# Kernel tuning notes

Measured on AMD Instinct MI355X. Metric: run time of the kernel, lower is better.

Reference implementation:

```python
import jax, jax.numpy as jnp
import numpy as np

INPUT_SIZE = 32
UNITS = 1024
T = 8192
N_MODULES = 2
INPUT_SCALING = 1.0
SPECTRAL_RADIUS = 0.99
LEAKY = 0.5
C_IN = 10
C_REC = 10


def _sparse_input_kernel(rng, M, N, C):
    # each row (input dim) projects to C random reservoir units, U(-1,1)
    W = np.zeros((M, N), dtype=np.float32)
    for i in range(M):
        idx = rng.choice(N, size=C, replace=False)
        W[i, idx] = rng.uniform(-1.0, 1.0, size=C).astype(np.float32)
    return W


def _sparse_recurrent_kernel(rng, M, C):
    # each column (unit) receives input from C random units, U(-1,1)
    W = np.zeros((M, M), dtype=np.float32)
    for i in range(M):
        idx = rng.choice(M, size=C, replace=False)
        W[idx, i] = rng.uniform(-1.0, 1.0, size=C).astype(np.float32)
    return W


def _make_recurrent(rng, M, leaky, rho):
    W = _sparse_recurrent_kernel(rng, M, C_REC)
    I = np.eye(M, dtype=np.float32)
    if leaky == 1:
        e = np.linalg.eigvals(W)
        W = W * (rho / np.max(np.abs(e)))
    else:
        W = W * leaky + I * (1.0 - leaky)
        e = np.linalg.eigvals(W)
        W = W * (rho / np.max(np.abs(e)))
        W = (W + I * (leaky - 1.0)) * (1.0 / leaky)
    return W.astype(np.float32)


def setup_inputs() -> dict:
    key = jax.random.key(0)
    rng = np.random.default_rng(0)
    u = jax.random.normal(key, (1, T, INPUT_SIZE), dtype=jnp.float32)
    # module 0: input_size -> units; module 1: units -> units
    kernel0 = jnp.asarray(_sparse_input_kernel(rng, INPUT_SIZE, UNITS, C_IN) * INPUT_SCALING)
    rec0 = jnp.asarray(_make_recurrent(rng, UNITS, LEAKY, SPECTRAL_RADIUS))
    bias0 = jnp.asarray(rng.uniform(-1.0, 1.0, size=UNITS).astype(np.float32))
    kernel1 = jnp.asarray(_sparse_input_kernel(rng, UNITS, UNITS, C_IN) * INPUT_SCALING)
    rec1 = jnp.asarray(_make_recurrent(rng, UNITS, LEAKY, SPECTRAL_RADIUS))
    bias1 = jnp.asarray(rng.uniform(-1.0, 1.0, size=UNITS).astype(np.float32))
    return {"u": u, "kernel0": kernel0, "rec0": rec0, "bias0": bias0,
            "kernel1": kernel1, "rec1": rec1, "bias1": bias1}


def _run_reservoir(u, K, W, b):
    # u: [B, T, in]; leaky-integrator ESN scan over time
    def step(h, ut):
        out = jnp.tanh(ut @ K + b + h @ W)
        h_new = h * (1.0 - LEAKY) + out * LEAKY
        return h_new, h_new
    h0 = jnp.zeros((u.shape[0], K.shape[1]), dtype=u.dtype)
    _, hs = jax.lax.scan(step, h0, jnp.swapaxes(u, 0, 1))  # [T, B, units]
    return jnp.swapaxes(hs, 0, 1)  # [B, T, units]


def reference(u, kernel0, rec0, bias0, kernel1, rec1, bias1):
    hs0 = _run_reservoir(u, kernel0, rec0, bias0)
    hs1 = _run_reservoir(hs0, kernel1, rec1, bias1)
    # deep reservoir output: concatenation of all module state sequences
    return jnp.concatenate([hs0, hs1], axis=-1)  # [1, T, 2*UNITS]
```

## Files before the change

kernel.cpp:

```cpp
#include <hip/hip_runtime.h>
#include <math.h>

typedef unsigned int uint;

#define T_STEPS 8192
#define R_CAP 10
#define K1_CAP 32
#define K0_CAP 6

__global__ __launch_bounds__(256) void prep_extract(
    const float* __restrict__ k0w, const float* __restrict__ r0w,
    const float* __restrict__ r1w, const float* __restrict__ k1w,
    float* __restrict__ r0vr, uint* __restrict__ r0ur, float* __restrict__ d0r,
    float* __restrict__ r1vr, uint* __restrict__ r1ur, float* __restrict__ d1r,
    float* __restrict__ k1vr, uint* __restrict__ k1ur, int* __restrict__ c1r,
    float* __restrict__ k0vr, uint* __restrict__ k0ur, int* __restrict__ c0r)
{
    int tid = blockIdx.x * 256 + threadIdx.x;
    int task = tid >> 10, j = tid & 1023;

    if (task <= 1) {
        const float* W = task ? r1w : r0w;
        float* vr = task ? r1vr : r0vr;
        uint*  ur = task ? r1ur : r0ur;
        float* dr = task ? d1r  : d0r;
        float diag = 0.f; int c = 0;
#pragma unroll 4
        for (int i = 0; i < 1024; ++i) {
            float v = W[i * 1024 + j];
            if (i == j) diag = v;
            else if (v != 0.f && c < R_CAP) {
                vr[j * R_CAP + c] = v; ur[j * R_CAP + c] = (uint)i; ++c;
            }
        }
        for (; c < R_CAP; ++c) { vr[j * R_CAP + c] = 0.f; ur[j * R_CAP + c] = 0u; }
        dr[j] = diag;
    } else if (task == 2) {
        int c = 0;
#pragma unroll 4
        for (int i = 0; i < 1024; ++i) {
            float v = k1w[i * 1024 + j];
            if (v != 0.f && c < K1_CAP) {
                k1vr[j * K1_CAP + c] = v; k1ur[j * K1_CAP + c] = (uint)i; ++c;
            }
        }
        c1r[j] = c;
        for (int q = c; q < K1_CAP; ++q) { k1vr[j * K1_CAP + q] = 0.f; k1ur[j * K1_CAP + q] = 0u; }
    } else {
        int c = 0;
        for (int i = 0; i < 32; ++i) {
            float v = k0w[i * 1024 + j];
            if (v != 0.f && c < K0_CAP) {
                k0vr[j * K0_CAP + c] = v; k0ur[j * K0_CAP + c] = (uint)i; ++c;
            }
        }
        c0r[j] = c;
        for (int q = c; q < K0_CAP; ++q) { k0vr[j * K0_CAP + q] = 0.f; k0ur[j * K0_CAP + q] = 0u; }
    }
}

__global__ __launch_bounds__(1024) void prep_slots(
    const float* __restrict__ r0vr, const uint* __restrict__ r0ur,
    const float* __restrict__ r1vr, const uint* __restrict__ r1ur,
    const float* __restrict__ k1vr, const uint* __restrict__ k1ur, const int* __restrict__ c1r,
    const float* __restrict__ k0vr, const uint* __restrict__ k0ur, const int* __restrict__ c0r,
    uint* __restrict__ Gr0a, float* __restrict__ Gr0v, int* __restrict__ Gcr0,
    uint* __restrict__ Gr1a, float* __restrict__ Gr1v, int* __restrict__ Gcr1,
    uint* __restrict__ Gk1a, float* __restrict__ Gk1v, int* __restrict__ Fc1,
    uint* __restrict__ Gk0a, float* __restrict__ Gk0v, int* __restrict__ Fc0,
    int* __restrict__ Fu1, int* __restrict__ Linv1)
{
    __shared__ int lc1[1024];
    __shared__ unsigned short sl1[1024];
    const int j = threadIdx.x;
    const int c1j = c1r[j], c0j = c0r[j];
    lc1[j] = c1j;
    __syncthreads();
    int s1 = 0;
#pragma unroll 4
    for (int i = 0; i < 1024; ++i) {
        int a = lc1[i]; s1 += (a < c1j) || (a == c1j && i < j);
    }
    sl1[j] = (unsigned short)s1;
    __syncthreads();

    {
        int n = 0;
        for (int k = 0; k < R_CAP; ++k) {
            float v = r0vr[j * R_CAP + k];
            uint  u = r0ur[j * R_CAP + k];
            Gr0v[j * R_CAP + k] = v;
            Gr0a[j * R_CAP + k] = (v != 0.f) ? (u << 2) : 0u;
            if (v != 0.f) n = k + 1;
        }
        Gcr0[j] = n;
        for (int k = 0; k < K0_CAP; ++k) {
            Gk0v[j * K0_CAP + k] = k0vr[j * K0_CAP + k];
            Gk0a[j * K0_CAP + k] = (k < c0j) ? (k0ur[j * K0_CAP + k] << 2) : 0u;
        }
        Fc0[j] = c0j;
    }
    {
        int n = 0;
        for (int k = 0; k < R_CAP; ++k) {
            float v = r1vr[j * R_CAP + k];
            uint  u = r1ur[j * R_CAP + k];
            Gr1v[s1 * R_CAP + k] = v;
            Gr1a[s1 * R_CAP + k] = (v != 0.f) ? (8192u + ((uint)sl1[u] << 2)) : 8192u;
            if (v != 0.f) n = k + 1;
        }
        Gcr1[s1] = n;
        for (int k = 0; k < K1_CAP; ++k) {
            Gk1v[s1 * K1_CAP + k] = k1vr[j * K1_CAP + k];
            Gk1a[s1 * K1_CAP + k] = (k < c1j) ? (k1ur[j * K1_CAP + k] << 2) : 0u;
        }
        Fc1[s1] = c1j; Fu1[s1] = j;
    }
    Linv1[j] = s1;
}

__global__ __launch_bounds__(256) void prep_greedy(
    const uint* __restrict__ Gr0a, const float* __restrict__ Gr0v, const int* __restrict__ Gcr0,
    const uint* __restrict__ Gr1a, const float* __restrict__ Gr1v, const int* __restrict__ Gcr1,
    const uint* __restrict__ Gk1a, const float* __restrict__ Gk1v, const int* __restrict__ Fc1,
    const uint* __restrict__ Gk0a, const float* __restrict__ Gk0v, const int* __restrict__ Fc0,
    float* __restrict__ Fr0v, uint* __restrict__ Fr0a,
    float* __restrict__ Fr1v, uint* __restrict__ Fr1a,
    float* __restrict__ Fk1v, uint* __restrict__ Fk1a,
    float* __restrict__ Fk0v, uint* __restrict__ Fk0a)
{
    __shared__ uint  ea[4][64][32];
    __shared__ float ev[4][64][32];
    __shared__ int   bl[4][64];
    const int wv   = threadIdx.x >> 6;
    const int lane = threadIdx.x & 63;
    const int half = (lane >> 5) * 32;
    const int gw   = blockIdx.x * 4 + wv;
    const int task = gw >> 4;
    const int col  = (gw & 15) * 64 + lane;

    const uint* ga; const float* gv; const int* gc; int cap;
    float* fv; uint* fa;
    if (task == 0)      { ga = Gr0a; gv = Gr0v; gc = Gcr0; cap = R_CAP;  fv = Fr0v; fa = Fr0a; }
    else if (task == 1) { ga = Gr1a; gv = Gr1v; gc = Gcr1; cap = R_CAP;  fv = Fr1v; fa = Fr1a; }
    else if (task == 2) { ga = Gk1a; gv = Gk1v; gc = Fc1;  cap = K1_CAP; fv = Fk1v; fa = Fk1a; }
    else                { ga = Gk0a; gv = Gk0v; gc = Fc0;  cap = K0_CAP; fv = Fk0v; fa = Fk0a; }

    const int cnt = gc[col];
    for (int s = 0; s < cap; ++s) {
        ea[wv][lane][s] = ga[col * cap + s];
        ev[wv][lane][s] = gv[col * cap + s];
    }
    __syncthreads();

    for (int slot = 0; slot < 32; ++slot) {
        bl[wv][lane] = 0;
        __syncthreads();
        int pick = -1;
        const bool active = (slot < cap) && (slot < cnt);
        for (int rnd = 0; rnd < 4; ++rnd) {
            if (active && pick < 0) {
                int best = slot, bload = 1 << 30;
                for (int e = slot; e < cnt; ++e) {
                    int b  = (int)((ea[wv][lane][e] >> 2) & 31u);
                    int ld = bl[wv][half + b];
                    if (ld < bload) { bload = ld; best = e; }
                }
                int bb = (int)((ea[wv][lane][best] >> 2) & 31u);
                if (rnd == 3) {
                    atomicAdd(&bl[wv][half + bb], 1); pick = best;
                } else {
                    int old = atomicAdd(&bl[wv][half + bb], 1);
                    if (old >= 1) atomicSub(&bl[wv][half + bb], 1);
                    else pick = best;
                }
            }
            __syncthreads();
        }
        if (active && pick > slot) {
            uint  ta = ea[wv][lane][slot]; ea[wv][lane][slot] = ea[wv][lane][pick]; ea[wv][lane][pick] = ta;
            float tv = ev[wv][lane][slot]; ev[wv][lane][slot] = ev[wv][lane][pick]; ev[wv][lane][pick] = tv;
        }
        __syncthreads();
    }

    for (int s = 0; s < cap; ++s) fv[col * cap + s] = ev[wv][lane][s];
    for (int p = 0; p < cap / 2; ++p)
        fa[col * (cap / 2) + p] = (ea[wv][lane][2 * p] & 0xffffu) | (ea[wv][lane][2 * p + 1] << 16);
}

__device__ __forceinline__ float fast_tanh(float x) {
    float ax = fabsf(x);
    float e  = __expf(-2.0f * ax);
    float r  = __builtin_amdgcn_rcpf(1.0f + e);
    float t  = (1.0f - e) * r;
    return copysignf(t, x);
}

#define LD(A) (*(const float*)(smem + (A)))

#define STEP(P, UOFF, DO1)                                                     \
  {                                                                            \
    float xa = __builtin_fmaf(d0, h0j, b0), xb = 0.f, xc = 0.f, xd = 0.f;      \
    {                                                                          \
      uint p0 = r0a[0], p1 = r0a[1], p2 = r0a[2], p3 = r0a[3], p4 = r0a[4];    \
      xa += r0v[0] * LD((p0 & 0xffffu) + (P) * 4096u);                         \
      xb += r0v[1] * LD((p0 >> 16)     + (P) * 4096u);                         \
      xc += r0v[2] * LD((p1 & 0xffffu) + (P) * 4096u);                         \
      xd += r0v[3] * LD((p1 >> 16)     + (P) * 4096u);                         \
      xa += r0v[4] * LD((p2 & 0xffffu) + (P) * 4096u);                         \
      xb += r0v[5] * LD((p2 >> 16)     + (P) * 4096u);                         \
      xc += r0v[6] * LD((p3 & 0xffffu) + (P) * 4096u);                         \
      xd += r0v[7] * LD((p3 >> 16)     + (P) * 4096u);                         \
      xa += r0v[8] * LD((p4 & 0xffffu) + (P) * 4096u);                         \
      xb += r0v[9] * LD((p4 >> 16)     + (P) * 4096u);                         \
    }                                                                          \
    _Pragma("unroll")                                                          \
    for (int kc = 0; kc < K0_CAP; kc += 2) {                                   \
      if (kc < k0m) {                                                          \
        uint pr = k0a[kc >> 1];                                                \
        xc += k0v[kc]     * LD((pr & 0xffffu) + (UOFF));                       \
        xd += k0v[kc + 1] * LD((pr >> 16)     + (UOFF));                       \
      }                                                                        \
    }                                                                          \
    float o0  = fast_tanh((xa + xb) + (xc + xd));                              \
    float h0n = 0.5f * (h0j + o0);                                             \
    ((float*)(smem + (1 - (P)) * 4096u))[j] = h0n;                             \
    *o0p = h0n; o0p += 2048;                                                   \
    __syncthreads();                                                           \
    float g1 = 0.f;                                                            \
    if (DO1) g1 = LD(8192u + (P) * 4096u + l1off);                             \
    float ya = __builtin_fmaf(d1, h1j, b1), yb = 0.f, yc = 0.f, yd = 0.f;      \
    _Pragma("unroll")                                                          \
    for (int kc = 0; kc < K1_CAP; kc += 4) {                                   \
      if (kc < k1m) {                                                          \
        uint pa = k1a[kc >> 1], pb = k1a[(kc >> 1) + 1];                       \
        ya += k1v[kc]     * LD((pa & 0xffffu) + (1 - (P)) * 4096u);            \
        yb += k1v[kc + 1] * LD((pa >> 16)     + (1 - (P)) * 4096u);            \
        yc += k1v[kc + 2] * LD((pb & 0xffffu) + (1 - (P)) * 4096u);            \
        yd += k1v[kc + 3] * LD((pb >> 16)     + (1 - (P)) * 4096u);            \
      }                                                                        \
    }                                                                          \
    {                                                                          \
      uint p0 = r1a[0], p1 = r1a[1], p2 = r1a[2], p3 = r1a[3], p4 = r1a[4];    \
      ya += r1v[0] * LD((p0 & 0xffffu) + (P) * 4096u);                         \
      yb += r1v[1] * LD((p0 >> 16)     + (P) * 4096u);                         \
      yc += r1v[2] * LD((p1 & 0xffffu) + (P) * 4096u);                         \
      yd += r1v[3] * LD((p1 >> 16)     + (P) * 4096u);                         \
      ya += r1v[4] * LD((p2 & 0xffffu) + (P) * 4096u);                         \
      yb += r1v[5] * LD((p2 >> 16)     + (P) * 4096u);                         \
      yc += r1v[6] * LD((p3 & 0xffffu) + (P) * 4096u);                         \
      yd += r1v[7] * LD((p3 >> 16)     + (P) * 4096u);                         \
      ya += r1v[8] * LD((p4 & 0xffffu) + (P) * 4096u);                         \
      yb += r1v[9] * LD((p4 >> 16)     + (P) * 4096u);                         \
    }                                                                          \
    if (DO1) { *o1p = g1; o1p += 2048; }                                       \
    float o1  = fast_tanh((ya + yb) + (yc + yd));                              \
    float h1n = 0.5f * (h1j + o1);                                             \
    ((float*)(smem + 8192u + (1 - (P)) * 4096u))[j] = h1n;                     \
    h0j = h0n; h1j = h1n;                                                      \
  }

__global__ __launch_bounds__(1024, 4) void reservoir_main(
    const float* __restrict__ u,
    const float* __restrict__ bias0, const float* __restrict__ bias1,
    const float* __restrict__ d0r, const float* __restrict__ d1r,
    const float* __restrict__ Fr0v, const uint* __restrict__ Fr0a,
    const float* __restrict__ Fr1v, const uint* __restrict__ Fr1a,
    const float* __restrict__ Fk1v, const uint* __restrict__ Fk1a,
    const float* __restrict__ Fk0v, const uint* __restrict__ Fk0a,
    const int* __restrict__ Fc1, const int* __restrict__ Fc0,
    const int* __restrict__ Fu1, const int* __restrict__ Linv1,
    float* __restrict__ out)
{
    __shared__ __align__(16) char smem[24576];
    const int j = threadIdx.x;

    float r0v[R_CAP], r1v[R_CAP], k1v[K1_CAP], k0v[K0_CAP];
    uint  r0a[R_CAP / 2], r1a[R_CAP / 2], k1a[K1_CAP / 2], k0a[K0_CAP / 2];
#pragma unroll
    for (int k = 0; k < R_CAP; ++k) { r0v[k] = Fr0v[j * R_CAP + k]; r1v[k] = Fr1v[j * R_CAP + k]; }
#pragma unroll
    for (int k = 0; k < R_CAP / 2; ++k) { r0a[k] = Fr0a[j * (R_CAP / 2) + k]; r1a[k] = Fr1a[j * (R_CAP / 2) + k]; }
#pragma unroll
    for (int k = 0; k < K1_CAP; ++k) k1v[k] = Fk1v[j * K1_CAP + k];
#pragma unroll
    for (int k = 0; k < K1_CAP / 2; ++k) k1a[k] = Fk1a[j * (K1_CAP / 2) + k];
#pragma unroll
    for (int k = 0; k < K0_CAP; ++k) k0v[k] = Fk0v[j * K0_CAP + k];
#pragma unroll
    for (int k = 0; k < K0_CAP / 2; ++k) k0a[k] = Fk0a[j * (K0_CAP / 2) + k];

    const int u1 = Fu1[j];
    const float b0 = bias0[j],  d0 = d0r[j];
    const float b1 = bias1[u1], d1 = d1r[u1];
    const uint l1off = (uint)(Linv1[j] << 2);
    float* o0p = out + j;
    float* o1p = out + 1024 + j;

    int k1m = Fc1[j], k0m = Fc0[j];
#pragma unroll
    for (int s = 32; s >= 1; s >>= 1) {
        int a = __shfl_xor(k1m, s, 64); k1m = a > k1m ? a : k1m;
        int b = __shfl_xor(k0m, s, 64); k0m = b > k0m ? b : k0m;
    }
    k1m = __builtin_amdgcn_readfirstlane((k1m + 3) & ~3);
    k0m = __builtin_amdgcn_readfirstlane((k0m + 1) & ~1);

    ((float*)(smem        ))[j] = 0.f;
    ((float*)(smem +  4096))[j] = 0.f;
    ((float*)(smem +  8192))[j] = 0.f;
    ((float*)(smem + 12288))[j] = 0.f;
    float h0j = 0.f, h1j = 0.f;

    {
        ((float*)(smem + 16384))[j]        = u[j];
        ((float*)(smem + 16384))[1024 + j] = u[1024 + j];
        __syncthreads();
        STEP(0, 16384u, 0)
        STEP(1, 16384u + 128u, 1)
    }
    for (int t = 2; t < T_STEPS; t += 2) {
        if ((t & 63) == 0) {
            ((float*)(smem + 16384))[j]        = u[t * 32 + j];
            ((float*)(smem + 16384))[1024 + j] = u[t * 32 + 1024 + j];
            __syncthreads();
        }
        uint uoff = 16384u + (uint)((t & 63) << 7);
        STEP(0, uoff, 1)
        STEP(1, uoff + 128u, 1)
    }
    __syncthreads();
    *o1p = LD(8192u + l1off);
}

extern "C" void kernel_launch(void* const* d_in, const int* in_sizes, int n_in,
                              void* d_out, int out_size, void* d_ws, size_t ws_size,
                              hipStream_t stream) {
    const float* u   = (const float*)d_in[0];
    const float* k0w = (const float*)d_in[1];
    const float* r0w = (const float*)d_in[2];
    const float* b0  = (const float*)d_in[3];
    const float* k1w = (const float*)d_in[4];
    const float* r1w = (const float*)d_in[5];
    const float* b1  = (const float*)d_in[6];
    float* out = (float*)d_out;

    char* w = (char*)d_ws;
    float* r0vr = (float*)w; w += 1024 * R_CAP * 4;
    uint*  r0ur = (uint*)w;  w += 1024 * R_CAP * 4;
    float* d0r  = (float*)w; w += 1024 * 4;
    float* r1vr = (float*)w; w += 1024 * R_CAP * 4;
    uint*  r1ur = (uint*)w;  w += 1024 * R_CAP * 4;
    float* d1r  = (float*)w; w += 1024 * 4;
    float* k1vr = (float*)w; w += 1024 * K1_CAP * 4;
    uint*  k1ur = (uint*)w;  w += 1024 * K1_CAP * 4;
    int*   c1r  = (int*)w;   w += 1024 * 4;
    float* k0vr = (float*)w; w += 1024 * K0_CAP * 4;
    uint*  k0ur = (uint*)w;  w += 1024 * K0_CAP * 4;
    int*   c0r  = (int*)w;   w += 1024 * 4;
    uint*  Gr0a = (uint*)w;  w += 1024 * R_CAP * 4;
    float* Gr0v = (float*)w; w += 1024 * R_CAP * 4;
    int*   Gcr0 = (int*)w;   w += 1024 * 4;
    uint*  Gr1a = (uint*)w;  w += 1024 * R_CAP * 4;
    float* Gr1v = (float*)w; w += 1024 * R_CAP * 4;
    int*   Gcr1 = (int*)w;   w += 1024 * 4;
    uint*  Gk1a = (uint*)w;  w += 1024 * K1_CAP * 4;
    float* Gk1v = (float*)w; w += 1024 * K1_CAP * 4;
    uint*  Gk0a = (uint*)w;  w += 1024 * K0_CAP * 4;
    float* Gk0v = (float*)w; w += 1024 * K0_CAP * 4;
    float* Fr0v = (float*)w; w += 1024 * R_CAP * 4;
    uint*  Fr0a = (uint*)w;  w += 1024 * (R_CAP / 2) * 4;
    float* Fr1v = (float*)w; w += 1024 * R_CAP * 4;
    uint*  Fr1a = (uint*)w;  w += 1024 * (R_CAP / 2) * 4;
    float* Fk1v = (float*)w; w += 1024 * K1_CAP * 4;
    uint*  Fk1a = (uint*)w;  w += 1024 * (K1_CAP / 2) * 4;
    float* Fk0v = (float*)w; w += 1024 * K0_CAP * 4;
    uint*  Fk0a = (uint*)w;  w += 1024 * (K0_CAP / 2) * 4;
    int*   Fc1  = (int*)w;   w += 1024 * 4;
    int*   Fc0  = (int*)w;   w += 1024 * 4;
    int*   Fu1  = (int*)w;   w += 1024 * 4;
    int*   Linv1 = (int*)w;

    prep_extract<<<16, 256, 0, stream>>>(k0w, r0w, r1w, k1w,
                                         r0vr, r0ur, d0r, r1vr, r1ur, d1r,
                                         k1vr, k1ur, c1r, k0vr, k0ur, c0r);
    prep_slots<<<1, 1024, 0, stream>>>(r0vr, r0ur, r1vr, r1ur,
                                       k1vr, k1ur, c1r, k0vr, k0ur, c0r,
                                       Gr0a, Gr0v, Gcr0, Gr1a, Gr1v, Gcr1,
                                       Gk1a, Gk1v, Fc1, Gk0a, Gk0v, Fc0,
                                       Fu1, Linv1);
    prep_greedy<<<16, 256, 0, stream>>>(Gr0a, Gr0v, Gcr0, Gr1a, Gr1v, Gcr1,
                                        Gk1a, Gk1v, Fc1, Gk0a, Gk0v, Fc0,
                                        Fr0v, Fr0a, Fr1v, Fr1a,
                                        Fk1v, Fk1a, Fk0v, Fk0a);
    reservoir_main<<<1, 1024, 0, stream>>>(u, b0, b1, d0r, d1r,
                                           Fr0v, Fr0a, Fr1v, Fr1a,
                                           Fk1v, Fk1a, Fk0v, Fk0a,
                                           Fc1, Fc0, Fu1, Linv1,
                                           out);
}
```

Baseline: 15.85 ms.

## Skew layer-1 by one step to use one barrier per timestep

The two reservoir layers are software-pipelined: layer 1 now computes step t-1 from the layer-0 state already published in the previous iteration, so layer 0 and layer 1 run in the same phase and each timestep needs only one block barrier instead of two. The barrier is also replaced by a lighter LDS-wait plus s_barrier with scheduling fences, avoiding the full waitcnt that __syncthreads emits. A drain iteration and an adjusted final store handle the one-step skew. This adds epilogue complexity and relies on the double-buffer indexing staying correct under the new ordering.

```diff
diff --git a/kernel.cpp b/kernel.cpp
--- a/kernel.cpp
+++ b/kernel.cpp
@@ -199,66 +199,85 @@
 
 #define LD(A) (*(const float*)(smem + (A)))
 
-#define STEP(P, UOFF, DO1)                                                     \
+#define SOFTBAR do {                                                           \
+    asm volatile("s_waitcnt lgkmcnt(0)" ::: "memory");                         \
+    __builtin_amdgcn_sched_barrier(0);                                         \
+    __builtin_amdgcn_s_barrier();                                              \
+    __builtin_amdgcn_sched_barrier(0);                                         \
+  } while (0)
+
+#define ITER(P, DO0, DO1, DOG, UOFF)                                           \
   {                                                                            \
-    float xa = __builtin_fmaf(d0, h0j, b0), xb = 0.f, xc = 0.f, xd = 0.f;      \
-    {                                                                          \
-      uint p0 = r0a[0], p1 = r0a[1], p2 = r0a[2], p3 = r0a[3], p4 = r0a[4];    \
-      xa += r0v[0] * LD((p0 & 0xffffu) + (P) * 4096u);                         \
-      xb += r0v[1] * LD((p0 >> 16)     + (P) * 4096u);                         \
-      xc += r0v[2] * LD((p1 & 0xffffu) + (P) * 4096u);                         \
-      xd += r0v[3] * LD((p1 >> 16)     + (P) * 4096u);                         \
-      xa += r0v[4] * LD((p2 & 0xffffu) + (P) * 4096u);                         \
-      xb += r0v[5] * LD((p2 >> 16)     + (P) * 4096u);                         \
-      xc += r0v[6] * LD((p3 & 0xffffu) + (P) * 4096u);                         \
-      xd += r0v[7] * LD((p3 >> 16)     + (P) * 4096u);                         \
-      xa += r0v[8] * LD((p4 & 0xffffu) + (P) * 4096u);                         \
-      xb += r0v[9] * LD((p4 >> 16)     + (P) * 4096u);                         \
+    float g1v = 0.f;                                                           \
+    if (DOG) g1v = LD(8192u + (P) * 4096u + l1off);                            \
+    if (DO0) {                                                                 \
+      float xa = __builtin_fmaf(d0, h0j, b0), xb = 0.f, xc = 0.f, xd = 0.f;    \
+      {                                                                        \
+        uint p0 = r0a[0], p1 = r0a[1], p2 = r0a[2], p3 = r0a[3], p4 = r0a[4];  \
+        xa += r0v[0] * LD((p0 & 0xffffu) + (P) * 4096u);                       \
+        xb += r0v[1] * LD((p0 >> 16)     + (P) * 4096u);                       \
+        xc += r0v[2] * LD((p1 & 0xffffu) + (P) * 4096u);                       \
+        xd += r0v[3] * LD((p1 >> 16)     + (P) * 4096u);                       \
+        xa += r0v[4] * LD((p2 & 0xffffu) + (P) * 4096u);                       \
+        xb += r0v[5] * LD((p2 >> 16)     + (P) * 4096u);                       \
+        xc += r0v[6] * LD((p3 & 0xffffu) + (P) * 4096u);                       \
+        xd += r0v[7] * LD((p3 >> 16)     + (P) * 4096u);                       \
+        xa += r0v[8] * LD((p4 & 0xffffu) + (P) * 4096u);                       \
+        xb += r0v[9] * LD((p4 >> 16)     + (P) * 4096u);                       \
+      }                                                                        \
+      _Pragma("unroll")                                                        \
+      for (int kc = 0; kc < K0_CAP; kc += 2) {                                 \
+        if (kc < k0m) {                                                        \
+          uint pr = k0a[kc >> 1];                                              \
+          xc += k0v[kc]     * LD((pr & 0xffffu) + (UOFF));                     \
+          xd += k0v[kc + 1] * LD((pr >> 16)     + (UOFF));                     \
+        }                                                                      \
+      }                                                                        \
+      float o0  = fast_tanh((xa + xb) + (xc + xd));                            \
+      float h0n = 0.5f * (h0j + o0);                                           \
+      ((float*)(smem + (1 - (P)) * 4096u))[j] = h0n;                           \
+      *o0p = h0n; o0p += 2048;                                                 \
+      h0j = h0n;                                                               \
     }                                                                          \
-    _Pragma("unroll")                                                          \
-    for (int kc = 0; kc < K0_CAP; kc += 2) {                                   \
-      if (kc < k0m) {                                                          \
-        uint pr = k0a[kc >> 1];                                                \
-        xc += k0v[kc]     * LD((pr & 0xffffu) + (UOFF));                       \
-        xd += k0v[kc + 1] * LD((pr >> 16)     + (UOFF));                       \
+    if (DOG) { *o1p = g1v; o1p += 2048; }                                      \
+    if (DO1) {                                                                 \
+      float ya = __builtin_fmaf(d1, h1j, b1), yb = 0.f, yc = 0.f, yd = 0.f;    \
+      _Pragma("unroll")                                                        \
+      for (int kc = 0; kc < K1_CAP; kc += 4) {                                 \
+        if (kc < k1m) {                                                        \
+          uint pa = k1a[kc >> 1], pb = k1a[(kc >> 1) + 1];                     \
+          ya += k1v[kc]     * LD((pa & 0xffffu) + (P) * 4096u);                \
+          yb += k1v[kc + 1] * LD((pa >> 16)     + (P) * 4096u);                \
+          yc += k1v[kc + 2] * LD((pb & 0xffffu) + (P) * 4096u);                \
+          yd += k1v[kc + 3] * LD((pb >> 16)     + (P) * 4096u);                \
+        }                                                                      \
       }                                                                        \
+      {                                                                        \
+        uint p0 = r1a[0], p1 = r1a[1], p2 = r1a[2], p3 = r1a[3], p4 = r1a[4];  \
+        ya += r1v[0] * LD((p0 & 0xffffu) + (P) * 4096u);                       \
+        yb += r1v[1] * LD((p0 >> 16)     + (P) * 4096u);                       \
+        yc += r1v[2] * LD((p1 & 0xffffu) + (P) * 4096u);                       \
+        yd += r1v[3] * LD((p1 >> 16)     + (P) * 4096u);                       \
+        ya += r1v[4] * LD((p2 & 0xffffu) + (P) * 4096u);                       \
+        yb += r1v[5] * LD((p2 >> 16)     + (P) * 4096u);                       \
+        yc += r1v[6] * LD((p3 & 0xffffu) + (P) * 4096u);                       \
+        yd += r1v[7] * LD((p3 >> 16)     + (P) * 4096u);                       \
+        ya += r1v[8] * LD((p4 & 0xffffu) + (P) * 4096u);                       \
+        yb += r1v[9] * LD((p4 >> 16)     + (P) * 4096u);                       \
+      }                                                                        \
+      float o1  = fast_tanh((ya + yb) + (yc + yd));                            \
+      float h1n = 0.5f * (h1j + o1);                                           \
+      ((float*)(smem + 8192u + (1 - (P)) * 4096u))[j] = h1n;                   \
+      h1j = h1n;                                                               \
     }                                                                          \
-    float o0  = fast_tanh((xa + xb) + (xc + xd));                              \
-    float h0n = 0.5f * (h0j + o0);                                             \
-    ((float*)(smem + (1 - (P)) * 4096u))[j] = h0n;                             \
-    *o0p = h0n; o0p += 2048;                                                   \
-    __syncthreads();                                                           \
-    float g1 = 0.f;                                                            \
-    if (DO1) g1 = LD(8192u + (P) * 4096u + l1off);                             \
-    float ya = __builtin_fmaf(d1, h1j, b1), yb = 0.f, yc = 0.f, yd = 0.f;      \
-    _Pragma("unroll")                                                          \
-    for (int kc = 0; kc < K1_CAP; kc += 4) {                                   \
-      if (kc < k1m) {                                                          \
-        uint pa = k1a[kc >> 1], pb = k1a[(kc >> 1) + 1];                       \
-        ya += k1v[kc]     * LD((pa & 0xffffu) + (1 - (P)) * 4096u);            \
-        yb += k1v[kc + 1] * LD((pa >> 16)     + (1 - (P)) * 4096u);            \
-        yc += k1v[kc + 2] * LD((pb & 0xffffu) + (1 - (P)) * 4096u);            \
-        yd += k1v[kc + 3] * LD((pb >> 16)     + (1 - (P)) * 4096u);            \
-      }                                                                        \
-    }                                                                          \
-    {                                                                          \
-      uint p0 = r1a[0], p1 = r1a[1], p2 = r1a[2], p3 = r1a[3], p4 = r1a[4];    \
-      ya += r1v[0] * LD((p0 & 0xffffu) + (P) * 4096u);                         \
-      yb += r1v[1] * LD((p0 >> 16)     + (P) * 4096u);                         \
-      yc += r1v[2] * LD((p1 & 0xffffu) + (P) * 4096u);                         \
-      yd += r1v[3] * LD((p1 >> 16)     + (P) * 4096u);                         \
-      ya += r1v[4] * LD((p2 & 0xffffu) + (P) * 4096u);                         \
-      yb += r1v[5] * LD((p2 >> 16)     + (P) * 4096u);                         \
-      yc += r1v[6] * LD((p3 & 0xffffu) + (P) * 4096u);                         \
-      yd += r1v[7] * LD((p3 >> 16)     + (P) * 4096u);                         \
-      ya += r1v[8] * LD((p4 & 0xffffu) + (P) * 4096u);                         \
-      yb += r1v[9] * LD((p4 >> 16)     + (P) * 4096u);                         \
-    }                                                                          \
-    if (DO1) { *o1p = g1; o1p += 2048; }                                       \
-    float o1  = fast_tanh((ya + yb) + (yc + yd));                              \
-    float h1n = 0.5f * (h1j + o1);                                             \
-    ((float*)(smem + 8192u + (1 - (P)) * 4096u))[j] = h1n;                     \
-    h0j = h0n; h1j = h1n;                                                      \
+    SOFTBAR;                                                                   \
+  }
+
+#define STAGE(TT)                                                              \
+  {                                                                            \
+    ((float*)(smem + 16384))[j]        = u[(TT) * 32 + j];                     \
+    ((float*)(smem + 16384))[1024 + j] = u[(TT) * 32 + 1024 + j];              \
+    SOFTBAR;                                                                   \
   }
 
 __global__ __launch_bounds__(1024, 4) void reservoir_main(
@@ -313,25 +332,18 @@
     ((float*)(smem + 12288))[j] = 0.f;
     float h0j = 0.f, h1j = 0.f;
 
-    {
-        ((float*)(smem + 16384))[j]        = u[j];
-        ((float*)(smem + 16384))[1024 + j] = u[1024 + j];
-        __syncthreads();
-        STEP(0, 16384u, 0)
-        STEP(1, 16384u + 128u, 1)
-    }
+    STAGE(0)
+    ITER(0, 1, 0, 0, 16384u)
+    ITER(1, 1, 1, 0, 16384u + 128u)
+
     for (int t = 2; t < T_STEPS; t += 2) {
-        if ((t & 63) == 0) {
-            ((float*)(smem + 16384))[j]        = u[t * 32 + j];
-            ((float*)(smem + 16384))[1024 + j] = u[t * 32 + 1024 + j];
-            __syncthreads();
-        }
+        if ((t & 63) == 0) STAGE(t)
         uint uoff = 16384u + (uint)((t & 63) << 7);
-        STEP(0, uoff, 1)
-        STEP(1, uoff + 128u, 1)
-    }
-    __syncthreads();
-    *o1p = LD(8192u + l1off);
+        ITER(0, 1, 1, 1, uoff)
+        ITER(1, 1, 1, 1, uoff + 128u)
+    }
+    ITER(0, 0, 1, 1, 16384u)
+    *o1p = LD(8192u + 4096u + l1off);
 }
 
 extern "C" void kernel_launch(void* const* d_in, const int* in_sizes, int n_in,
```

Measured after the change: 17.41 ms. 1.1x slower.
